# Optimization experiments

Measured on AMD Instinct MI355X. Metric: run time of the kernel, lower is better.

## Reference

```python
import jax, jax.numpy as jnp
import numpy as np

# dims
B, N, FN, FE, H, OUT, MP = 128, 64, 64, 16, 128, 32, 4
P_EDGE = 0.125  # avg degree ~8


def _build_graph_indices():
    """Replicates the torch index construction (nonzero / per-row cat loops)
    with vectorized numpy; done once at setup since adjacency is an input."""
    rng = np.random.default_rng(0)
    up = np.triu(rng.random((B, N, N)) < P_EDGE, 1)
    A = (up | up.transpose(0, 2, 1)).astype(np.int64)  # symmetric, no self-loops
    b_idx, n_idx, nhb_idx = np.nonzero(A)              # row-major, like torch nonzero
    E = b_idx.shape[0]
    ids = np.zeros_like(A)
    ids[b_idx, n_idx, nhb_idx] = np.arange(E) + 1      # adj_of_edge_batch_indices
    deg = A.sum(-1)                                    # [B,N]
    edge_deg = deg[b_idx, nhb_idx]                     # in-degree of each edge's neighbour
    rows = ids[b_idx, nhb_idx, :]                      # [E,N]
    eb = rows[rows > 0] - 1                            # ingoing edge ids, per-row order
    igeb = np.repeat(np.arange(E), edge_deg)           # receiving edge id
    keep = n_idx[igeb] != nhb_idx[eb]                  # drop the reverse edge
    eb, igeb = eb[keep], igeb[keep]
    node_mask = deg != 0                               # [B,N]
    return A, b_idx, n_idx, nhb_idx, eb, igeb, node_mask


def setup_inputs() -> dict:
    key = jax.random.key(0)
    ks = jax.random.split(key, 9)
    A, b_idx, n_idx, nhb_idx, eb, igeb, node_mask = _build_graph_indices()
    s = lambda k, *sh: jax.random.normal(k, sh, jnp.float32) * 0.05
    return {
        "nodes": jax.random.normal(ks[0], (B, N, FN), jnp.float32),
        "edges": jax.random.normal(ks[1], (B, N, N, FE), jnp.float32),
        "W_emb": s(ks[2], FN + FN + FE, H),
        "b_emb": jnp.zeros((H,), jnp.float32),
        "W_msg": s(ks[3], H, H),
        "W_edge": s(ks[4], H, H),
        "b_prop": jnp.zeros((H,), jnp.float32),
        "W_out": s(ks[5], H, OUT),
        "b_out": jnp.zeros((OUT,), jnp.float32),
        "edges_b_idx": jnp.asarray(b_idx),
        "edges_n_idx": jnp.asarray(n_idx),
        "edges_nhb_idx": jnp.asarray(nhb_idx),
        "ing_eb_idx": jnp.asarray(eb),
        "ing_igeb_idx": jnp.asarray(igeb),
        "node_mask": jnp.asarray(node_mask),
    }


def reference(nodes, edges, W_emb, b_emb, W_msg, W_edge, b_prop, W_out, b_out,
              edges_b_idx, edges_n_idx, edges_nhb_idx, ing_eb_idx, ing_igeb_idx,
              node_mask):
    E = edges_b_idx.shape[0]
    Bn, Nn = nodes.shape[0], nodes.shape[1]
    # preprocess_edges: tanh(Linear([node; neighbour; edge]))
    cat = jnp.concatenate([
        nodes[edges_b_idx, edges_n_idx],      # [E,FN]
        nodes[edges_b_idx, edges_nhb_idx],    # [E,FN]
        edges[edges_b_idx, edges_n_idx, edges_nhb_idx],  # [E,FE]
    ], axis=-1)
    e_feat = jnp.tanh(cat @ W_emb + b_emb)    # [E,H]
    # edge-memory message passing; scatter(set)+masked sum == segment_sum over
    # the filtered ingoing-edge pairs (unset slots are zero in the original)
    mem = jnp.zeros((E, W_emb.shape[1]), cat.dtype)
    for _ in range(MP):
        msg = jax.ops.segment_sum(mem[ing_eb_idx], ing_igeb_idx, num_segments=E)
        mem = jnp.tanh(msg @ W_msg + e_feat @ W_edge + b_prop)
    # node_sets scatter + sum over degree slots == segment_sum per receiving node
    node_seg = edges_b_idx * Nn + edges_n_idx
    graph_sets = jax.ops.segment_sum(mem, node_seg, num_segments=Bn * Nn)
    graph_sets = graph_sets.reshape(Bn, Nn, -1)   # [B,N,H]
    # readout: masked sum over nodes, then linear
    g = (graph_sets * node_mask[..., None].astype(cat.dtype)).sum(1)  # [B,H]
    return g @ W_out + b_out
```

## Files before the change

kernel.cpp:

```cpp
#include <hip/hip_runtime.h>
#include <hip/hip_bf16.h>

#define NB 128
#define NN 64
#define HH 128

typedef short bf16x8 __attribute__((ext_vector_type(8)));
typedef float f32x4 __attribute__((ext_vector_type(4)));

static inline int cdiv(int a, int b) { return (a + b - 1) / b; }

__device__ __forceinline__ float tanh_fast(float x) {
    float ax = fabsf(x);
    float ex = __expf(-2.0f * ax);
    float t  = (1.0f - ex) / (1.0f + ex);
    return copysignf(t, x);
}

__device__ __forceinline__ unsigned short f2bfs(float f) {
    unsigned u; __builtin_memcpy(&u, &f, 4);
    u = (u + 0x7FFFu + ((u >> 16) & 1u)) >> 16;
    return (unsigned short)u;
}
__device__ __forceinline__ float bfs2f(unsigned short s) {
    unsigned u = ((unsigned)s) << 16;
    float f; __builtin_memcpy(&f, &u, 4);
    return f;
}
__device__ __forceinline__ int pack2(unsigned short a, unsigned short b) {
    return (int)((unsigned)a | ((unsigned)b << 16));
}
__device__ __forceinline__ f32x4 mfma16(bf16x8 a, bf16x8 b, f32x4 c) {
    return __builtin_amdgcn_mfma_f32_16x16x32_bf16(a, b, c, 0, 0, 0);
}

__global__ void scatter_ids_kernel(const int* __restrict__ bI, const int* __restrict__ nI,
                                   const int* __restrict__ nhI, int* __restrict__ idmat, int E) {
    int e = blockIdx.x * blockDim.x + threadIdx.x;
    if (e >= E) return;
    idmat[((bI[e] << 6) + nI[e]) * NN + nhI[e]] = e;
}
__global__ void build_rev_kernel(const int* __restrict__ bI, const int* __restrict__ nI,
                                 const int* __restrict__ nhI, const int* __restrict__ idmat,
                                 int* __restrict__ rev, int E) {
    int e = blockIdx.x * blockDim.x + threadIdx.x;
    if (e >= E) return;
    rev[e] = idmat[((bI[e] << 6) + nhI[e]) * NN + nI[e]];
}
__global__ void build_ptr_kernel(const int* __restrict__ bI, const int* __restrict__ nI,
                                 int E, int* __restrict__ ptr) {
    int v = blockIdx.x * blockDim.x + threadIdx.x;
    if (v > NB * NN) return;
    int lo = 0, hi = E;
    while (lo < hi) {
        int mid = (lo + hi) >> 1;
        int sg = (bI[mid] << 6) + nI[mid];
        if (sg < v) lo = mid + 1; else hi = mid;
    }
    ptr[v] = lo;
}
__global__ void prep_w_kernel(const float* __restrict__ W_emb, const float* __restrict__ W_edge,
                              const float* __restrict__ W_msg,
                              unsigned short* __restrict__ WTe, unsigned short* __restrict__ WTd,
                              unsigned short* __restrict__ WTm, float* __restrict__ g) {
    int i = blockIdx.x * blockDim.x + threadIdx.x;
    if (i < 128 * 160) { int c = i / 160, k = i % 160;
        WTe[c * 160 + k] = f2bfs(k < 144 ? W_emb[k * 128 + c] : 0.f); return; }
    i -= 128 * 160;
    if (i < 128 * 128) { int c = i >> 7, k = i & 127;
        WTd[c * 128 + k] = f2bfs(W_edge[k * 128 + c]); return; }
    i -= 128 * 128;
    if (i < 128 * 128) { int c = i >> 7, k = i & 127;
        WTm[c * 128 + k] = f2bfs(W_msg[k * 128 + c]); return; }
    i -= 128 * 128;
    if (i < NB * HH) g[i] = 0.f;
}

__global__ __launch_bounds__(256) void g01_kernel(
    const float* __restrict__ nodes, const float* __restrict__ edgesF,
    const unsigned short* __restrict__ WTe, const unsigned short* __restrict__ WTd,
    const float* __restrict__ b_emb, const float* __restrict__ b_prop,
    const int* __restrict__ bI, const int* __restrict__ nI, const int* __restrict__ nhI,
    float* __restrict__ ef2, unsigned short* __restrict__ mem1, int E)
{
    __shared__ __align__(16) char lds[51200];
    unsigned short* A = (unsigned short*)lds;
    const int tid = threadIdx.x;
    const int e0  = blockIdx.x * 64;

    for (int s = tid; s < 1280; s += 256) {
        int row = s / 20, kg = s % 20, k0 = kg * 8;
        int e = e0 + row;
        float f0=0,f1=0,f2=0,f3=0,f4=0,f5=0,f6=0,f7=0;
        if (e < E && k0 < 144) {
            int b = bI[e], n = nI[e], nh = nhI[e];
            const float* p;
            if (k0 < 64)        p = nodes  + ((((size_t)b << 6) + n)  << 6) + k0;
            else if (k0 < 128)  p = nodes  + ((((size_t)b << 6) + nh) << 6) + (k0 - 64);
            else                p = edgesF + ((((((size_t)b << 6) + n) << 6) + nh) << 4) + (k0 - 128);
            float4 x = *(const float4*)p, y = *(const float4*)(p + 4);
            f0=x.x; f1=x.y; f2=x.z; f3=x.w; f4=y.x; f5=y.y; f6=y.z; f7=y.w;
        }
        int4 w;
        w.x = pack2(f2bfs(f0), f2bfs(f1)); w.y = pack2(f2bfs(f2), f2bfs(f3));
        w.z = pack2(f2bfs(f4), f2bfs(f5)); w.w = pack2(f2bfs(f6), f2bfs(f7));
        *(int4*)&A[row * 168 + k0] = w;
    }
    __syncthreads();

    const int lane = tid & 63, wid = tid >> 6;
    const int wm = wid & 1, wn = wid >> 1;
    const int l15 = lane & 15, lk = lane >> 4;
    const int r0 = wm * 32, cb = wn * 64;

    f32x4 acc[2][4];
    #pragma unroll
    for (int mi = 0; mi < 2; ++mi)
        #pragma unroll
        for (int ni = 0; ni < 4; ++ni) acc[mi][ni] = (f32x4)0.f;

    #pragma unroll
    for (int ks = 0; ks < 5; ++ks) {
        bf16x8 a0 = *(const bf16x8*)&A[(r0 + l15)      * 168 + ks * 32 + lk * 8];
        bf16x8 a1 = *(const bf16x8*)&A[(r0 + 16 + l15) * 168 + ks * 32 + lk * 8];
        #pragma unroll
        for (int ni = 0; ni < 4; ++ni) {
            bf16x8 bb = *(const bf16x8*)&WTe[(size_t)(cb + ni * 16 + l15) * 160 + ks * 32 + lk * 8];
            acc[0][ni] = mfma16(a0, bb, acc[0][ni]);
            acc[1][ni] = mfma16(a1, bb, acc[1][ni]);
        }
    }
    __syncthreads();

    unsigned short* T = (unsigned short*)lds;
    #pragma unroll
    for (int mi = 0; mi < 2; ++mi)
        #pragma unroll
        for (int ni = 0; ni < 4; ++ni) {
            int col = cb + ni * 16 + l15;
            float be = b_emb[col];
            #pragma unroll
            for (int j = 0; j < 4; ++j) {
                int row = r0 + mi * 16 + lk * 4 + j;
                T[row * 136 + col] = f2bfs(tanh_fast(acc[mi][ni][j] + be));
            }
        }
    __syncthreads();

    f32x4 acc2[2][4];
    #pragma unroll
    for (int mi = 0; mi < 2; ++mi)
        #pragma unroll
        for (int ni = 0; ni < 4; ++ni) acc2[mi][ni] = (f32x4)0.f;

    #pragma unroll
    for (int ks = 0; ks < 4; ++ks) {
        bf16x8 a0 = *(const bf16x8*)&T[(r0 + l15)      * 136 + ks * 32 + lk * 8];
        bf16x8 a1 = *(const bf16x8*)&T[(r0 + 16 + l15) * 136 + ks * 32 + lk * 8];
        #pragma unroll
        for (int ni = 0; ni < 4; ++ni) {
            bf16x8 bb = *(const bf16x8*)&WTd[(size_t)(cb + ni * 16 + l15) * 128 + ks * 32 + lk * 8];
            acc2[0][ni] = mfma16(a0, bb, acc2[0][ni]);
            acc2[1][ni] = mfma16(a1, bb, acc2[1][ni]);
        }
    }
    __syncthreads();

    float*          EF = (float*)lds;
    unsigned short* MB = (unsigned short*)(lds + 64 * 132 * 4);
    #pragma unroll
    for (int mi = 0; mi < 2; ++mi)
        #pragma unroll
        for (int ni = 0; ni < 4; ++ni) {
            int col = cb + ni * 16 + l15;
            float bp = b_prop[col];
            #pragma unroll
            for (int j = 0; j < 4; ++j) {
                int row = r0 + mi * 16 + lk * 4 + j;
                float z = acc2[mi][ni][j] + bp;
                EF[row * 132 + col] = z;
                MB[row * 136 + col] = f2bfs(tanh_fast(z));
            }
        }
    __syncthreads();
    for (int s = tid; s < 2048; s += 256) {
        int row = s >> 5, c0 = (s & 31) * 4, e = e0 + row;
        if (e < E) *(float4*)&ef2[(size_t)e * HH + c0] = *(const float4*)&EF[row * 132 + c0];
    }
    for (int s = tid; s < 1024; s += 256) {
        int row = s >> 4, c0 = (s & 15) * 8, e = e0 + row;
        if (e < E) *(int4*)&mem1[(size_t)e * HH + c0] = *(const int4*)&MB[row * 136 + c0];
    }
}

template <int LAST>
__global__ __launch_bounds__(64) void mp_kernel(
    const unsigned short* __restrict__ memIn, const float* __restrict__ ef2,
    const unsigned short* __restrict__ WTm, const int* __restrict__ rev,
    const int* __restrict__ ptr, unsigned short* __restrict__ memOut,
    float* __restrict__ g)
{
    const int u = blockIdx.x;
    const int s = ptr[u], e1 = ptr[u + 1];
    const int deg = e1 - s;
    if (deg == 0) return;

    __shared__ __align__(16) char ldsu[16 * 132 * 4];
    __shared__ float Srow[128];
    __shared__ int   rvls[16];
    unsigned short* A = (unsigned short*)ldsu;
    float*          C = (float*)ldsu;

    const int lane = threadIdx.x;
    const int l15 = lane & 15, lk = lane >> 4;

    {
        const int m0 = min(deg, 16);
        #pragma unroll
        for (int ii = 0; ii < 4; ++ii) {
            int sl = lane + ii * 64;
            int r = sl >> 4, k0 = (sl & 15) * 8;
            int4 w = make_int4(0, 0, 0, 0);
            if (r < m0) w = *(const int4*)&memIn[(size_t)(s + r) * HH + k0];
            *(int4*)&A[r * 136 + k0] = w;
        }
    }
    __syncthreads();

    {
        float s0 = 0.f, s1 = 0.f;
        const int m0 = min(deg, 16);
        for (int r = 0; r < m0; ++r) {
            s0 += bfs2f(A[r * 136 + lane]);
            s1 += bfs2f(A[r * 136 + lane + 64]);
        }
        for (int r = 16; r < deg; ++r) {
            s0 += bfs2f(memIn[(size_t)(s + r) * HH + lane]);
            s1 += bfs2f(memIn[(size_t)(s + r) * HH + lane + 64]);
        }
        Srow[lane] = s0; Srow[lane + 64] = s1;
    }

    float ga0 = 0.f, ga1 = 0.f;

    for (int c0 = 0; c0 < deg; c0 += 16) {
        const int nrows = min(16, deg - c0);
        if (c0) {
            __syncthreads();
            #pragma unroll
            for (int ii = 0; ii < 4; ++ii) {
                int sl = lane + ii * 64;
                int r = sl >> 4, k0 = (sl & 15) * 8;
                int4 w = make_int4(0, 0, 0, 0);
                if (r < nrows) w = *(const int4*)&memIn[(size_t)(s + c0 + r) * HH + k0];
                *(int4*)&A[r * 136 + k0] = w;
            }
        }
        if (lane < nrows) rvls[lane] = rev[s + c0 + lane];
        __syncthreads();

        #pragma unroll
        for (int ii = 0; ii < 4; ++ii) {
            int sl = lane + ii * 64;
            int r = sl >> 4, k0 = (sl & 15) * 8;
            int4 w = *(const int4*)&A[r * 136 + k0];
            unsigned short hs[8];
            #pragma unroll
            for (int q = 0; q < 4; ++q) {
                int raw = (&w.x)[q];
                float lo = bfs2f((unsigned short)(raw & 0xFFFF));
                float hi = bfs2f((unsigned short)((unsigned)raw >> 16));
                hs[2 * q]     = f2bfs(Srow[k0 + 2 * q]     - lo);
                hs[2 * q + 1] = f2bfs(Srow[k0 + 2 * q + 1] - hi);
            }
            int4 o;
            o.x = pack2(hs[0], hs[1]); o.y = pack2(hs[2], hs[3]);
            o.z = pack2(hs[4], hs[5]); o.w = pack2(hs[6], hs[7]);
            *(int4*)&A[r * 136 + k0] = o;
        }
        __syncthreads();

        f32x4 acc[8];
        #pragma unroll
        for (int ni = 0; ni < 8; ++ni) acc[ni] = (f32x4)0.f;
        #pragma unroll
        for (int ks = 0; ks < 4; ++ks) {
            bf16x8 a = *(const bf16x8*)&A[l15 * 136 + ks * 32 + lk * 8];
            #pragma unroll
            for (int ni = 0; ni < 8; ++ni) {
                bf16x8 bb = *(const bf16x8*)&WTm[(size_t)(ni * 16 + l15) * HH + ks * 32 + lk * 8];
                acc[ni] = mfma16(a, bb, acc[ni]);
            }
        }
        __syncthreads();

        #pragma unroll
        for (int ni = 0; ni < 8; ++ni)
            #pragma unroll
            for (int j = 0; j < 4; ++j)
                C[(lk * 4 + j) * 132 + ni * 16 + l15] = acc[ni][j];
        __syncthreads();

        if (!LAST) {
            #pragma unroll
            for (int ii = 0; ii < 4; ++ii) {
                int sl = lane + ii * 64;
                int r = sl >> 4, k0 = (sl & 15) * 8;
                if (r < nrows) {
                    int rv = rvls[r];
                    const float* ep = &ef2[(size_t)rv * HH + k0];
                    float4 f0 = *(const float4*)ep, f1 = *(const float4*)(ep + 4);
                    const float* cp = &C[r * 132 + k0];
                    unsigned short hs[8];
                    hs[0] = f2bfs(tanh_fast(cp[0] + f0.x)); hs[1] = f2bfs(tanh_fast(cp[1] + f0.y));
                    hs[2] = f2bfs(tanh_fast(cp[2] + f0.z)); hs[3] = f2bfs(tanh_fast(cp[3] + f0.w));
                    hs[4] = f2bfs(tanh_fast(cp[4] + f1.x)); hs[5] = f2bfs(tanh_fast(cp[5] + f1.y));
                    hs[6] = f2bfs(tanh_fast(cp[6] + f1.z)); hs[7] = f2bfs(tanh_fast(cp[7] + f1.w));
                    int4 o;
                    o.x = pack2(hs[0], hs[1]); o.y = pack2(hs[2], hs[3]);
                    o.z = pack2(hs[4], hs[5]); o.w = pack2(hs[6], hs[7]);
                    *(int4*)&memOut[(size_t)rv * HH + k0] = o;
                }
            }
        } else {
            for (int r = 0; r < nrows; ++r) {
                int rv = rvls[r];
                ga0 += tanh_fast(C[r * 132 + lane]      + ef2[(size_t)rv * HH + lane]);
                ga1 += tanh_fast(C[r * 132 + lane + 64] + ef2[(size_t)rv * HH + lane + 64]);
            }
        }
    }

    if (LAST) {
        const int b = u >> 6;
        atomicAdd(&g[(size_t)b * HH + lane],      ga0);
        atomicAdd(&g[(size_t)b * HH + lane + 64], ga1);
    }
}

__global__ void out2_kernel(const float* __restrict__ g, const float* __restrict__ W_out,
                            const float* __restrict__ b_out, float* __restrict__ out) {
    int b = blockIdx.x, tid = threadIdx.x;
    if (tid < 32) {
        float a = b_out[tid];
        for (int h = 0; h < HH; ++h) a += g[(size_t)b * HH + h] * W_out[h * 32 + tid];
        out[b * 32 + tid] = a;
    }
}

extern "C" void kernel_launch(void* const* d_in, const int* in_sizes, int n_in,
                              void* d_out, int out_size, void* d_ws, size_t ws_size,
                              hipStream_t stream) {
    const float* nodes  = (const float*)d_in[0];
    const float* edgesF = (const float*)d_in[1];
    const float* W_emb  = (const float*)d_in[2];
    const float* b_emb  = (const float*)d_in[3];
    const float* W_msg  = (const float*)d_in[4];
    const float* W_edge = (const float*)d_in[5];
    const float* b_prop = (const float*)d_in[6];
    const float* W_out  = (const float*)d_in[7];
    const float* b_out  = (const float*)d_in[8];
    const int*   bI     = (const int*)d_in[9];
    const int*   nI     = (const int*)d_in[10];
    const int*   nhI    = (const int*)d_in[11];
    const int    E      = in_sizes[9];
    float*       out    = (float*)d_out;

    char* ws = (char*)d_ws;
    size_t al = 255;
    size_t szEf  = (((size_t)E * HH * 4) + al) & ~al;
    size_t szMem = (((size_t)E * HH * 2) + al) & ~al;
    size_t szI   = (((size_t)E * 4) + al) & ~al;
    float*          ef2   = (float*)ws;                      ws += szEf;
    unsigned short* memA  = (unsigned short*)ws;             ws += szMem;
    unsigned short* memB  = (unsigned short*)ws;             ws += szMem;
    float*          g     = (float*)ws;                      ws += (size_t)NB * HH * 4;
    int*            idmat = (int*)ws;                        ws += (size_t)NB * NN * NN * 4;
    int*            rev   = (int*)ws;                        ws += szI;
    int*            ptr   = (int*)ws;                        ws += (((size_t)(NB * NN + 1) * 4) + al) & ~al;
    unsigned short* WTe   = (unsigned short*)ws;             ws += 128 * 160 * 2;
    unsigned short* WTd   = (unsigned short*)ws;             ws += 128 * 128 * 2;
    unsigned short* WTm   = (unsigned short*)ws;             ws += 128 * 128 * 2;

    scatter_ids_kernel<<<cdiv(E, 256), 256, 0, stream>>>(bI, nI, nhI, idmat, E);
    build_rev_kernel  <<<cdiv(E, 256), 256, 0, stream>>>(bI, nI, nhI, idmat, rev, E);
    build_ptr_kernel  <<<cdiv(NB * NN + 1, 256), 256, 0, stream>>>(bI, nI, E, ptr);
    prep_w_kernel     <<<cdiv(128 * 160 + 2 * 128 * 128 + NB * HH, 256), 256, 0, stream>>>(
                        W_emb, W_edge, W_msg, WTe, WTd, WTm, g);

    const int gb = cdiv(E, 64);
    g01_kernel<<<gb, 256, 0, stream>>>(nodes, edgesF, WTe, WTd, b_emb, b_prop,
                                       bI, nI, nhI, ef2, memA, E);
    mp_kernel<0><<<NB * NN, 64, 0, stream>>>(memA, ef2, WTm, rev, ptr, memB, nullptr);
    mp_kernel<0><<<NB * NN, 64, 0, stream>>>(memB, ef2, WTm, rev, ptr, memA, nullptr);
    mp_kernel<1><<<NB * NN, 64, 0, stream>>>(memA, ef2, WTm, rev, ptr, nullptr, g);

    out2_kernel<<<NB, 64, 0, stream>>>(g, W_out, b_out, out);
}
```

Measured before the change: 286.9 us.

## Pack four nodes per block and build MFMA operands directly in registers

The message-passing kernel now handles four destination nodes per 256-thread block, one wavefront each, instead of one node per 64-thread block. It also drops the shared-memory staging of edge rows and the C tile: each lane loads its memIn row, subtracts it from the node sum in registers, and feeds the result as the MFMA B operand with WTm as the A operand. The tanh epilogue then reads the accumulators directly. This removes most barriers and LDS round trips and cuts the launch to a quarter of the blocks. In exchange, the last pass does 32 atomics per lane group after shuffle reductions, and a wave with deg==0 returns early while its block-mates continue.

```diff
diff --git a/kernel.cpp b/kernel.cpp
--- a/kernel.cpp
+++ b/kernel.cpp
@@ -194,147 +194,132 @@
 }
 
 template <int LAST>
-__global__ __launch_bounds__(64) void mp_kernel(
+__global__ __launch_bounds__(256) void mp_kernel(
     const unsigned short* __restrict__ memIn, const float* __restrict__ ef2,
     const unsigned short* __restrict__ WTm, const int* __restrict__ rev,
     const int* __restrict__ ptr, unsigned short* __restrict__ memOut,
     float* __restrict__ g)
 {
-    const int u = blockIdx.x;
-    const int s = ptr[u], e1 = ptr[u + 1];
+    const int wv   = threadIdx.x >> 6;
+    const int u    = (blockIdx.x << 2) + wv;
+    const int lane = threadIdx.x & 63;
+    const int l15  = lane & 15, lk = lane >> 4;
+
+    __shared__ float Sall[4][132];
+    float* S = Sall[wv];
+
+    const int s   = ptr[u], e1 = ptr[u + 1];
     const int deg = e1 - s;
     if (deg == 0) return;
 
-    __shared__ __align__(16) char ldsu[16 * 132 * 4];
-    __shared__ float Srow[128];
-    __shared__ int   rvls[16];
-    unsigned short* A = (unsigned short*)ldsu;
-    float*          C = (float*)ldsu;
-
-    const int lane = threadIdx.x;
-    const int l15 = lane & 15, lk = lane >> 4;
-
-    {
-        const int m0 = min(deg, 16);
-        #pragma unroll
-        for (int ii = 0; ii < 4; ++ii) {
-            int sl = lane + ii * 64;
-            int r = sl >> 4, k0 = (sl & 15) * 8;
-            int4 w = make_int4(0, 0, 0, 0);
-            if (r < m0) w = *(const int4*)&memIn[(size_t)(s + r) * HH + k0];
-            *(int4*)&A[r * 136 + k0] = w;
-        }
-    }
-    __syncthreads();
-
     {
         float s0 = 0.f, s1 = 0.f;
-        const int m0 = min(deg, 16);
-        for (int r = 0; r < m0; ++r) {
-            s0 += bfs2f(A[r * 136 + lane]);
-            s1 += bfs2f(A[r * 136 + lane + 64]);
-        }
-        for (int r = 16; r < deg; ++r) {
+        for (int r = 0; r < deg; ++r) {
             s0 += bfs2f(memIn[(size_t)(s + r) * HH + lane]);
             s1 += bfs2f(memIn[(size_t)(s + r) * HH + lane + 64]);
         }
-        Srow[lane] = s0; Srow[lane + 64] = s1;
-    }
-
-    float ga0 = 0.f, ga1 = 0.f;
+        S[lane] = s0; S[lane + 64] = s1;
+    }
+    __threadfence_block();
+
+    float gacc[8][4];
+    if (LAST) {
+        #pragma unroll
+        for (int ni = 0; ni < 8; ++ni)
+            #pragma unroll
+            for (int j = 0; j < 4; ++j) gacc[ni][j] = 0.f;
+    }
 
     for (int c0 = 0; c0 < deg; c0 += 16) {
-        const int nrows = min(16, deg - c0);
-        if (c0) {
-            __syncthreads();
-            #pragma unroll
-            for (int ii = 0; ii < 4; ++ii) {
-                int sl = lane + ii * 64;
-                int r = sl >> 4, k0 = (sl & 15) * 8;
-                int4 w = make_int4(0, 0, 0, 0);
-                if (r < nrows) w = *(const int4*)&memIn[(size_t)(s + c0 + r) * HH + k0];
-                *(int4*)&A[r * 136 + k0] = w;
-            }
-        }
-        if (lane < nrows) rvls[lane] = rev[s + c0 + lane];
-        __syncthreads();
-
-        #pragma unroll
-        for (int ii = 0; ii < 4; ++ii) {
-            int sl = lane + ii * 64;
-            int r = sl >> 4, k0 = (sl & 15) * 8;
-            int4 w = *(const int4*)&A[r * 136 + k0];
-            unsigned short hs[8];
-            #pragma unroll
-            for (int q = 0; q < 4; ++q) {
-                int raw = (&w.x)[q];
-                float lo = bfs2f((unsigned short)(raw & 0xFFFF));
-                float hi = bfs2f((unsigned short)((unsigned)raw >> 16));
-                hs[2 * q]     = f2bfs(Srow[k0 + 2 * q]     - lo);
-                hs[2 * q + 1] = f2bfs(Srow[k0 + 2 * q + 1] - hi);
-            }
-            int4 o;
-            o.x = pack2(hs[0], hs[1]); o.y = pack2(hs[2], hs[3]);
-            o.z = pack2(hs[4], hs[5]); o.w = pack2(hs[6], hs[7]);
-            *(int4*)&A[r * 136 + k0] = o;
-        }
-        __syncthreads();
+        const int  nrows = min(16, deg - c0);
+        const bool valid = (l15 < nrows);
+        const int  erow  = s + c0 + l15;
+        const int  rv    = valid ? rev[erow] : 0;
 
         f32x4 acc[8];
         #pragma unroll
         for (int ni = 0; ni < 8; ++ni) acc[ni] = (f32x4)0.f;
+
         #pragma unroll
         for (int ks = 0; ks < 4; ++ks) {
-            bf16x8 a = *(const bf16x8*)&A[l15 * 136 + ks * 32 + lk * 8];
+            bf16x8 bfrag;
+            {
+                float4 sa = *(const float4*)&S[ks * 32 + lk * 8];
+                float4 sb = *(const float4*)&S[ks * 32 + lk * 8 + 4];
+                int4 mr = make_int4(0, 0, 0, 0);
+                if (valid) mr = *(const int4*)&memIn[(size_t)erow * HH + ks * 32 + lk * 8];
+                unsigned short h[8];
+                #pragma unroll
+                for (int q = 0; q < 4; ++q) {
+                    int raw = (&mr.x)[q];
+                    float lo = bfs2f((unsigned short)(raw & 0xFFFF));
+                    float hi = bfs2f((unsigned short)((unsigned)raw >> 16));
+                    float sv0 = (q < 2) ? ((q == 0) ? sa.x : sa.z) : ((q == 2) ? sb.x : sb.z);
+                    float sv1 = (q < 2) ? ((q == 0) ? sa.y : sa.w) : ((q == 2) ? sb.y : sb.w);
+                    h[2 * q]     = f2bfs(sv0 - lo);
+                    h[2 * q + 1] = f2bfs(sv1 - hi);
+                }
+                #pragma unroll
+                for (int q = 0; q < 8; ++q) bfrag[q] = (short)h[q];
+                if (!valid) {
+                    #pragma unroll
+                    for (int q = 0; q < 8; ++q) bfrag[q] = 0;
+                }
+            }
             #pragma unroll
             for (int ni = 0; ni < 8; ++ni) {
-                bf16x8 bb = *(const bf16x8*)&WTm[(size_t)(ni * 16 + l15) * HH + ks * 32 + lk * 8];
-                acc[ni] = mfma16(a, bb, acc[ni]);
-            }
-        }
-        __syncthreads();
-
+                bf16x8 afrag = *(const bf16x8*)&WTm[(size_t)(ni * 16 + l15) * HH + ks * 32 + lk * 8];
+                acc[ni] = mfma16(afrag, bfrag, acc[ni]);
+            }
+        }
+
+        if (valid) {
+            if (!LAST) {
+                #pragma unroll
+                for (int ni = 0; ni < 8; ++ni) {
+                    int f0 = ni * 16 + lk * 4;
+                    float4 ef = *(const float4*)&ef2[(size_t)rv * HH + f0];
+                    unsigned short h0 = f2bfs(tanh_fast(acc[ni][0] + ef.x));
+                    unsigned short h1 = f2bfs(tanh_fast(acc[ni][1] + ef.y));
+                    unsigned short h2 = f2bfs(tanh_fast(acc[ni][2] + ef.z));
+                    unsigned short h3 = f2bfs(tanh_fast(acc[ni][3] + ef.w));
+                    uint2 o;
+                    o.x = (unsigned)pack2(h0, h1);
+                    o.y = (unsigned)pack2(h2, h3);
+                    *(uint2*)&memOut[(size_t)rv * HH + f0] = o;
+                }
+            } else {
+                #pragma unroll
+                for (int ni = 0; ni < 8; ++ni) {
+                    int f0 = ni * 16 + lk * 4;
+                    float4 ef = *(const float4*)&ef2[(size_t)rv * HH + f0];
+                    gacc[ni][0] += tanh_fast(acc[ni][0] + ef.x);
+                    gacc[ni][1] += tanh_fast(acc[ni][1] + ef.y);
+                    gacc[ni][2] += tanh_fast(acc[ni][2] + ef.z);
+                    gacc[ni][3] += tanh_fast(acc[ni][3] + ef.w);
+                }
+            }
+        }
+    }
+
+    if (LAST) {
         #pragma unroll
         for (int ni = 0; ni < 8; ++ni)
             #pragma unroll
-            for (int j = 0; j < 4; ++j)
-                C[(lk * 4 + j) * 132 + ni * 16 + l15] = acc[ni][j];
-        __syncthreads();
-
-        if (!LAST) {
-            #pragma unroll
-            for (int ii = 0; ii < 4; ++ii) {
-                int sl = lane + ii * 64;
-                int r = sl >> 4, k0 = (sl & 15) * 8;
-                if (r < nrows) {
-                    int rv = rvls[r];
-                    const float* ep = &ef2[(size_t)rv * HH + k0];
-                    float4 f0 = *(const float4*)ep, f1 = *(const float4*)(ep + 4);
-                    const float* cp = &C[r * 132 + k0];
-                    unsigned short hs[8];
-                    hs[0] = f2bfs(tanh_fast(cp[0] + f0.x)); hs[1] = f2bfs(tanh_fast(cp[1] + f0.y));
-                    hs[2] = f2bfs(tanh_fast(cp[2] + f0.z)); hs[3] = f2bfs(tanh_fast(cp[3] + f0.w));
-                    hs[4] = f2bfs(tanh_fast(cp[4] + f1.x)); hs[5] = f2bfs(tanh_fast(cp[5] + f1.y));
-                    hs[6] = f2bfs(tanh_fast(cp[6] + f1.z)); hs[7] = f2bfs(tanh_fast(cp[7] + f1.w));
-                    int4 o;
-                    o.x = pack2(hs[0], hs[1]); o.y = pack2(hs[2], hs[3]);
-                    o.z = pack2(hs[4], hs[5]); o.w = pack2(hs[6], hs[7]);
-                    *(int4*)&memOut[(size_t)rv * HH + k0] = o;
-                }
-            }
-        } else {
-            for (int r = 0; r < nrows; ++r) {
-                int rv = rvls[r];
-                ga0 += tanh_fast(C[r * 132 + lane]      + ef2[(size_t)rv * HH + lane]);
-                ga1 += tanh_fast(C[r * 132 + lane + 64] + ef2[(size_t)rv * HH + lane + 64]);
-            }
-        }
-    }
-
-    if (LAST) {
-        const int b = u >> 6;
-        atomicAdd(&g[(size_t)b * HH + lane],      ga0);
-        atomicAdd(&g[(size_t)b * HH + lane + 64], ga1);
+            for (int j = 0; j < 4; ++j) {
+                float v = gacc[ni][j];
+                v += __shfl_xor(v, 1); v += __shfl_xor(v, 2);
+                v += __shfl_xor(v, 4); v += __shfl_xor(v, 8);
+                gacc[ni][j] = v;
+            }
+        if (l15 == 0) {
+            const int b = u >> 6;
+            #pragma unroll
+            for (int ni = 0; ni < 8; ++ni)
+                #pragma unroll
+                for (int j = 0; j < 4; ++j)
+                    atomicAdd(&g[(size_t)b * HH + ni * 16 + lk * 4 + j], gacc[ni][j]);
+        }
     }
 }
 
@@ -391,9 +376,9 @@
     const int gb = cdiv(E, 64);
     g01_kernel<<<gb, 256, 0, stream>>>(nodes, edgesF, WTe, WTd, b_emb, b_prop,
                                        bI, nI, nhI, ef2, memA, E);
-    mp_kernel<0><<<NB * NN, 64, 0, stream>>>(memA, ef2, WTm, rev, ptr, memB, nullptr);
-    mp_kernel<0><<<NB * NN, 64, 0, stream>>>(memB, ef2, WTm, rev, ptr, memA, nullptr);
-    mp_kernel<1><<<NB * NN, 64, 0, stream>>>(memA, ef2, WTm, rev, ptr, nullptr, g);
+    mp_kernel<0><<<NB * NN / 4, 256, 0, stream>>>(memA, ef2, WTm, rev, ptr, memB, nullptr);
+    mp_kernel<0><<<NB * NN / 4, 256, 0, stream>>>(memB, ef2, WTm, rev, ptr, memA, nullptr);
+    mp_kernel<1><<<NB * NN / 4, 256, 0, stream>>>(memA, ef2, WTm, rev, ptr, nullptr, g);
 
     out2_kernel<<<NB, 64, 0, stream>>>(g, W_out, b_out, out);
 }
```

New measurement: 405.9 us. 1.41x slower.
